# Performance work log

Hardware: AMD Instinct MI355X
Metric: run time of the kernel (lower is better)

Reference implementation:

```python
import jax, jax.numpy as jnp
import numpy as np

N_NODES = 50000
N_RAND_EDGES = 800000
N_GRAPHS = 16
F_IN = 128
HID = 64
EMB = 16


def gat_layer(x, src, dst, W, a_src, a_dst, bias, heads, out_ch, concat):
    # x: [N, Fin]; W: [Fin, heads*out_ch]; a_src/a_dst: [heads, out_ch]
    n = x.shape[0]
    h = (x @ W).reshape(n, heads, out_ch)                      # [N, H, C]
    alpha_src = jnp.sum(h * a_src, axis=-1)                    # [N, H]
    alpha_dst = jnp.sum(h * a_dst, axis=-1)                    # [N, H]
    logits = jax.nn.leaky_relu(alpha_src[src] + alpha_dst[dst], 0.2)  # [E, H]
    # segment softmax over incoming edges of each dst node
    m = jax.ops.segment_max(logits, dst, num_segments=n)       # [N, H]
    e = jnp.exp(logits - m[dst])                               # [E, H]
    s = jax.ops.segment_sum(e, dst, num_segments=n)            # [N, H]
    alpha = e / (s[dst] + 1e-16)                               # [E, H]
    msg = h[src] * alpha[:, :, None]                           # [E, H, C]
    out = jax.ops.segment_sum(msg, dst, num_segments=n)        # [N, H, C]
    out = out.reshape(n, heads * out_ch) if concat else out.mean(axis=1)
    return out + bias, alpha


def setup_inputs() -> dict:
    key = jax.random.key(0)
    ks = jax.random.split(key, 20)
    x = jax.random.normal(ks[0], (N_NODES, F_IN), dtype=jnp.float32)
    src = jax.random.randint(ks[1], (N_RAND_EDGES,), 0, N_NODES)
    dst = jax.random.randint(ks[2], (N_RAND_EDGES,), 0, N_NODES)
    loops = jnp.arange(N_NODES)
    edge_index = jnp.stack([jnp.concatenate([src, loops]),
                            jnp.concatenate([dst, loops])]).astype(jnp.int64)
    batch = jnp.sort(jax.random.randint(ks[3], (N_NODES,), 0, N_GRAPHS)).astype(jnp.int64)
    p = lambda k, shp: (jax.random.normal(k, shp, dtype=jnp.float32) * 0.1)
    return {
        "x": x, "edge_index": edge_index, "batch": batch,
        # conv1: 128 -> 64, heads=2, concat -> 128
        "W1": p(ks[4], (F_IN, 2 * HID)), "as1": p(ks[5], (2, HID)), "ad1": p(ks[6], (2, HID)), "b1": p(ks[7], (2 * HID,)),
        # conv2: 128 -> 128, heads=1, mean
        "W2": p(ks[8], (2 * HID, 2 * HID)), "as2": p(ks[9], (1, 2 * HID)), "ad2": p(ks[10], (1, 2 * HID)), "b2": p(ks[11], (2 * HID,)),
        # conv3: 128 -> 16, heads=1, mean
        "W3": p(ks[12], (2 * HID, EMB)), "as3": p(ks[13], (1, EMB)), "ad3": p(ks[14], (1, EMB)), "b3": p(ks[15], (EMB,)),
        # final classifier 16 -> 2
        "Wl": p(ks[16], (EMB, 2)), "bl": p(ks[17], (2,)),
    }


def reference(x, edge_index, batch, W1, as1, ad1, b1, W2, as2, ad2, b2,
              W3, as3, ad3, b3, Wl, bl):
    src, dst = edge_index[0], edge_index[1]
    h1, a1 = gat_layer(x, src, dst, W1, as1, ad1, b1, heads=2, out_ch=HID, concat=True)
    h1 = jax.nn.relu(h1)
    h2, a2 = gat_layer(h1, src, dst, W2, as2, ad2, b2, heads=1, out_ch=2 * HID, concat=False)
    h2 = jax.nn.relu(h2)
    emb, a3 = gat_layer(h2, src, dst, W3, as3, ad3, b3, heads=1, out_ch=EMB, concat=False)
    # global mean pool over graphs (eval mode -> dropout is identity)
    counts = jax.ops.segment_sum(jnp.ones((emb.shape[0],), emb.dtype), batch, num_segments=N_GRAPHS)
    g_emb = jax.ops.segment_sum(emb, batch, num_segments=N_GRAPHS) / jnp.clip(counts, 1.0, None)[:, None]
    out = g_emb @ Wl + bl
    return (out, g_emb, emb, a1, a2, a3)
```

## Files before the change

### kernel.cpp

```cpp
#include <hip/hip_runtime.h>
#include <hip/hip_bf16.h>

#define DEVFN __device__ __forceinline__

using short8 = __attribute__((ext_vector_type(8))) short;
using f32x4  = __attribute__((ext_vector_type(4))) float;

DEVFN float ldf(const void* p, size_t i, bool f32) {
    return f32 ? ((const float*)p)[i]
               : __bfloat162float(((const __hip_bfloat16*)p)[i]);
}
DEVFN int ldidx(const void* p, size_t i, bool i64) {
    return i64 ? (int)((const long long*)p)[i] : ((const int*)p)[i];
}
DEVFN void stf(void* p, size_t i, float v, bool f32) {
    if (f32) ((float*)p)[i] = v;
    else     ((__hip_bfloat16*)p)[i] = __float2bfloat16(v);
}
DEVFN float lky(float v) { return v > 0.f ? v : 0.2f * v; }

DEVFN float bfbits2f(short s) {
    return __uint_as_float(((unsigned)(unsigned short)s) << 16);
}
DEVFN short f2bfbits(float f) {
    unsigned u = __float_as_uint(f);
    return (short)((u + 0x7fffu + ((u >> 16) & 1u)) >> 16);
}

__global__ void detect_k(const void* x, const void* ei, int* flags) {
    if (threadIdx.x == 0 && blockIdx.x == 0) {
        const __hip_bfloat16* xb = (const __hip_bfloat16*)x;
        int bad = 0;
        for (int i = 0; i < 512; ++i) {
            float v = __bfloat162float(xb[i]);
            if (!(v == v) || fabsf(v) > 1.0e6f) bad++;
        }
        flags[0] = (bad > 16) ? 1 : 0;
        const unsigned* w = (const unsigned*)ei;
        int zeros = 0;
        for (int i = 0; i < 64; ++i) if (w[2 * i + 1] == 0u) zeros++;
        flags[1] = (zeros >= 60) ? 1 : 0;
    }
}

__global__ void zero_i32(int* __restrict__ p, int n) {
    int i = blockIdx.x * blockDim.x + threadIdx.x;
    int st = gridDim.x * blockDim.x;
    for (; i < n; i += st) p[i] = 0;
}
__global__ void zero_f32(float* __restrict__ p, long n) {
    long i = (long)blockIdx.x * blockDim.x + threadIdx.x;
    long st = (long)gridDim.x * blockDim.x;
    for (; i < n; i += st) p[i] = 0.f;
}

__global__ void hist_k(const void* __restrict__ ei, int E, int* __restrict__ cnt,
                       const int* __restrict__ flags) {
    const bool i64 = flags[1] != 0;
    int e = blockIdx.x * blockDim.x + threadIdx.x;
    if (e >= E) return;
    atomicAdd(&cnt[ldidx(ei, (size_t)E + e, i64)], 1);
}

__global__ void scan_block_k(const int* __restrict__ cnt, int* __restrict__ incl,
                             int* __restrict__ part, int N) {
    __shared__ int sm[256];
    int tid = threadIdx.x;
    int i = blockIdx.x * 256 + tid;
    int v = (i < N) ? cnt[i] : 0;
    sm[tid] = v;
    __syncthreads();
    for (int o = 1; o < 256; o <<= 1) {
        int t = (tid >= o) ? sm[tid - o] : 0;
        __syncthreads();
        sm[tid] += t;
        __syncthreads();
    }
    if (i < N) incl[i] = sm[tid];
    if (tid == 255) part[blockIdx.x] = sm[255];
}

__global__ void scan_part_k(int* __restrict__ part, int nb) {
    __shared__ int sm[256];
    __shared__ int off;
    int tid = threadIdx.x;
    if (tid == 0) off = 0;
    __syncthreads();
    for (int b = 0; b < nb; b += 256) {
        int i = b + tid;
        int v = (i < nb) ? part[i] : 0;
        sm[tid] = v;
        __syncthreads();
        for (int o = 1; o < 256; o <<= 1) {
            int t = (tid >= o) ? sm[tid - o] : 0;
            __syncthreads();
            sm[tid] += t;
            __syncthreads();
        }
        if (i < nb) part[i] = sm[tid] - v + off;
        __syncthreads();
        if (tid == 255) off += sm[255];
        __syncthreads();
    }
}

__global__ void finalize_scan_k(int* __restrict__ incl_cur, const int* __restrict__ cnt,
                                const int* __restrict__ part, int* __restrict__ rs,
                                int N, int E) {
    int i = blockIdx.x * 256 + threadIdx.x;
    if (i >= N) return;
    int v = incl_cur[i] - cnt[i] + part[blockIdx.x];
    rs[i] = v;
    incl_cur[i] = v;
    if (i == N - 1) rs[N] = E;
}

__global__ void scatter_csr_k(const void* __restrict__ ei, int E, int* __restrict__ cur,
                              int2* __restrict__ csr, const int* __restrict__ flags) {
    const bool i64 = flags[1] != 0;
    int e = blockIdx.x * blockDim.x + threadIdx.x;
    if (e >= E) return;
    int s = ldidx(ei, e, i64);
    int d = ldidx(ei, (size_t)E + e, i64);
    int p = atomicAdd(&cur[d], 1);
    csr[p] = make_int2(s, e);
}

template <int DSRC, int FOUT, int HEADS>
__global__ __launch_bounds__(256) void gemm_alpha_mfma_k(
    const void* __restrict__ xin, const void* __restrict__ Wv,
    const void* __restrict__ asv, const void* __restrict__ adv,
    short* __restrict__ h_bf, float* __restrict__ as_out, float* __restrict__ ad_out,
    int N, const int* __restrict__ flags)
{
    constexpr int FIN = 128;
    constexpr int NCT = FOUT / 16;
    constexpr int CPH = FOUT / HEADS;
    constexpr int CTPH = CPH / 16;
    const bool f32 = flags[0] != 0;

    __shared__ short Wt[FOUT * FIN];

    for (int i = threadIdx.x; i < FIN * FOUT; i += 256) {
        int k = i / FOUT, c = i - (i / FOUT) * FOUT;
        short w;
        if (f32) w = f2bfbits(((const float*)Wv)[i]);
        else     w = ((const short*)Wv)[i];
        *(short*)((char*)Wt + (size_t)c * (FIN * 2) + (((k * 2) ^ ((c & 7) << 4)))) = w;
    }
    __syncthreads();

    const int wv = threadIdx.x >> 6;
    const int lane = threadIdx.x & 63;
    const int m0 = blockIdx.x * 64 + wv * 16;
    if (m0 >= N) return;
    const int lrow = lane & 15;
    const int lk   = lane >> 4;

    short8 afrag[4];
    if (DSRC == 0 && f32) {
        const float* xf = (const float*)xin + (size_t)(m0 + lrow) * FIN + lk * 8;
#pragma unroll
        for (int ks = 0; ks < 4; ++ks) {
            short8 t;
#pragma unroll
            for (int j = 0; j < 8; ++j) t[j] = f2bfbits(xf[ks * 32 + j]);
            afrag[ks] = t;
        }
    } else {
        const short* xb = (const short*)xin + (size_t)(m0 + lrow) * FIN + lk * 8;
#pragma unroll
        for (int ks = 0; ks < 4; ++ks)
            afrag[ks] = *(const short8*)(xb + ks * 32);
    }

    float csA[HEADS][4], cdA[HEADS][4];
#pragma unroll
    for (int hd = 0; hd < HEADS; ++hd)
#pragma unroll
        for (int r = 0; r < 4; ++r) { csA[hd][r] = 0.f; cdA[hd][r] = 0.f; }

#pragma unroll
    for (int ct = 0; ct < NCT; ++ct) {
        const int col = ct * 16 + lrow;
        const int hd = ct / CTPH;
        f32x4 acc = {0.f, 0.f, 0.f, 0.f};
#pragma unroll
        for (int ks = 0; ks < 4; ++ks) {
            const int kbyte = ks * 64 + lk * 16;
            short8 bfrag = *(const short8*)((const char*)Wt +
                               (size_t)col * (FIN * 2) + (kbyte ^ ((col & 7) << 4)));
            acc = __builtin_amdgcn_mfma_f32_16x16x32_bf16(afrag[ks], bfrag, acc, 0, 0, 0);
        }
        const float asc = ldf(asv, col, f32);
        const float adc = ldf(adv, col, f32);
#pragma unroll
        for (int r = 0; r < 4; ++r) {
            h_bf[(size_t)(m0 + lk * 4 + r) * FOUT + col] = f2bfbits(acc[r]);
            csA[hd][r] += acc[r] * asc;
            cdA[hd][r] += acc[r] * adc;
        }
    }

#pragma unroll
    for (int hd = 0; hd < HEADS; ++hd)
#pragma unroll
        for (int r = 0; r < 4; ++r) {
            float cs = csA[hd][r], cd = cdA[hd][r];
            for (int o = 1; o < 16; o <<= 1) {
                cs += __shfl_xor(cs, o);
                cd += __shfl_xor(cd, o);
            }
            csA[hd][r] = cs; cdA[hd][r] = cd;
        }
    if (lrow == 0) {
#pragma unroll
        for (int r = 0; r < 4; ++r) {
            int n = m0 + lk * 4 + r;
#pragma unroll
            for (int hd = 0; hd < HEADS; ++hd) {
                as_out[(size_t)n * HEADS + hd] = csA[hd][r];
                ad_out[(size_t)n * HEADS + hd] = cdA[hd][r];
            }
        }
    }
}

template <int HEADS>
__global__ __launch_bounds__(256) void softmax_csr_k(
    const float* __restrict__ as_, const float* __restrict__ ad_,
    const int* __restrict__ rs, const int2* __restrict__ csr,
    float* __restrict__ alpha_csr, void* __restrict__ dout, size_t aoff,
    int N, const int* __restrict__ flags)
{
    const bool f32 = flags[0] != 0;
    const int wid = (blockIdx.x * 256 + threadIdx.x) >> 6;
    const int lane = threadIdx.x & 63;
    if (wid >= N) return;
    const int beg = rs[wid], end = rs[wid + 1];
    const int deg = end - beg;

    const float ad0 = ad_[(size_t)wid * HEADS];
    const float ad1 = (HEADS == 2) ? ad_[(size_t)wid * HEADS + 1] : 0.f;

    if (deg <= 64) {
        const bool act = lane < deg;
        int2 se = make_int2(0, 0);
        if (act) se = csr[beg + lane];
        float l0 = act ? lky(as_[(size_t)se.x * HEADS] + ad0) : -1e30f;
        float l1 = 0.f;
        if (HEADS == 2) l1 = act ? lky(as_[(size_t)se.x * HEADS + 1] + ad1) : -1e30f;

        float m0 = l0, m1 = l1;
        for (int o = 1; o < 64; o <<= 1) {
            m0 = fmaxf(m0, __shfl_xor(m0, o));
            if (HEADS == 2) m1 = fmaxf(m1, __shfl_xor(m1, o));
        }
        float e0 = act ? expf(l0 - m0) : 0.f;
        float e1 = (HEADS == 2) ? (act ? expf(l1 - m1) : 0.f) : 0.f;
        float s0 = e0, s1 = e1;
        for (int o = 1; o < 64; o <<= 1) {
            s0 += __shfl_xor(s0, o);
            if (HEADS == 2) s1 += __shfl_xor(s1, o);
        }
        if (act) {
            const int p = beg + lane;
            float a0 = e0 * (1.f / (s0 + 1e-16f));
            alpha_csr[(size_t)p * HEADS] = a0;
            stf(dout, aoff + (size_t)se.y * HEADS, a0, f32);
            if (HEADS == 2) {
                float a1 = e1 * (1.f / (s1 + 1e-16f));
                alpha_csr[(size_t)p * 2 + 1] = a1;
                stf(dout, aoff + (size_t)se.y * 2 + 1, a1, f32);
            }
        }
        return;
    }

    float m0 = -1e30f, m1 = -1e30f;
    for (int p = beg + lane; p < end; p += 64) {
        int s = csr[p].x;
        m0 = fmaxf(m0, lky(as_[(size_t)s * HEADS] + ad0));
        if (HEADS == 2) m1 = fmaxf(m1, lky(as_[(size_t)s * HEADS + 1] + ad1));
    }
    for (int o = 1; o < 64; o <<= 1) {
        m0 = fmaxf(m0, __shfl_xor(m0, o));
        if (HEADS == 2) m1 = fmaxf(m1, __shfl_xor(m1, o));
    }
    float s0 = 0.f, s1 = 0.f;
    for (int p = beg + lane; p < end; p += 64) {
        int s = csr[p].x;
        s0 += expf(lky(as_[(size_t)s * HEADS] + ad0) - m0);
        if (HEADS == 2) s1 += expf(lky(as_[(size_t)s * HEADS + 1] + ad1) - m1);
    }
    for (int o = 1; o < 64; o <<= 1) {
        s0 += __shfl_xor(s0, o);
        if (HEADS == 2) s1 += __shfl_xor(s1, o);
    }
    const float inv0 = 1.f / (s0 + 1e-16f);
    const float inv1 = 1.f / (s1 + 1e-16f);

    for (int p = beg + lane; p < end; p += 64) {
        int2 se = csr[p];
        int s = se.x, eid = se.y;
        float a0 = expf(lky(as_[(size_t)s * HEADS] + ad0) - m0) * inv0;
        alpha_csr[(size_t)p * HEADS] = a0;
        stf(dout, aoff + (size_t)eid * HEADS, a0, f32);
        if (HEADS == 2) {
            float a1 = expf(lky(as_[(size_t)s * HEADS + 1] + ad1) - m1) * inv1;
            alpha_csr[(size_t)p * 2 + 1] = a1;
            stf(dout, aoff + (size_t)eid * 2 + 1, a1, f32);
        }
    }
}

template <int HEADS, bool RELU>
__global__ __launch_bounds__(256) void pull128_v3_k(
    const short* __restrict__ h_bf, const float* __restrict__ alpha_csr,
    const int* __restrict__ rs, const int2* __restrict__ csr,
    const void* __restrict__ bias, short* __restrict__ z_bf,
    int N, const int* __restrict__ flags)
{
    const bool f32 = flags[0] != 0;
    const int wid = (blockIdx.x * 256 + threadIdx.x) >> 6;
    if (wid >= N) return;
    const int lane = threadIdx.x & 63;
    const int cg = lane & 15;
    const int es = lane >> 4;
    const int h = (HEADS == 2) ? (cg >> 3) : 0;
    const int beg = rs[wid], end = rs[wid + 1];

    float acc[8] = {0.f, 0.f, 0.f, 0.f, 0.f, 0.f, 0.f, 0.f};
    for (int base = beg; base < end; base += 8) {
        const int pA = base + es;
        const int pB = base + 4 + es;
        int sA = 0, sB = 0;
        float aA = 0.f, aB = 0.f;
        if (pA < end) { sA = csr[pA].x; aA = alpha_csr[(size_t)pA * HEADS + h]; }
        if (pB < end) { sB = csr[pB].x; aB = alpha_csr[(size_t)pB * HEADS + h]; }
        const short8 hA = *(const short8*)(h_bf + (size_t)sA * 128 + cg * 8);
        const short8 hB = *(const short8*)(h_bf + (size_t)sB * 128 + cg * 8);
#pragma unroll
        for (int j = 0; j < 8; ++j)
            acc[j] = fmaf(bfbits2f(hA[j]), aA, acc[j]);
#pragma unroll
        for (int j = 0; j < 8; ++j)
            acc[j] = fmaf(bfbits2f(hB[j]), aB, acc[j]);
    }
#pragma unroll
    for (int j = 0; j < 8; ++j) {
        acc[j] += __shfl_xor(acc[j], 16);
        acc[j] += __shfl_xor(acc[j], 32);
    }
    if (es == 0) {
        short8 outv;
#pragma unroll
        for (int j = 0; j < 8; ++j) {
            float v = acc[j] + ldf(bias, cg * 8 + j, f32);
            if (RELU) v = fmaxf(v, 0.f);
            outv[j] = f2bfbits(v);
        }
        *(short8*)(z_bf + (size_t)wid * 128 + cg * 8) = outv;
    }
}

__global__ __launch_bounds__(256) void pull16_v2_k(
    const short* __restrict__ h_bf, const float* __restrict__ alpha_csr,
    const int* __restrict__ rs, const int2* __restrict__ csr,
    float* __restrict__ out, int N)
{
    const int wid = (blockIdx.x * 256 + threadIdx.x) >> 6;
    if (wid >= N) return;
    const int lane = threadIdx.x & 63;
    const int cg = lane & 7;
    const int es = lane >> 3;
    const int beg = rs[wid], end = rs[wid + 1];

    float a0 = 0.f, a1 = 0.f;
    for (int base = beg; base < end; base += 8) {
        const int p = base + es;
        if (p < end) {
            const int sj = csr[p].x;
            const float a = alpha_csr[p];
            const int hv = *(const int*)(h_bf + (size_t)sj * 16 + cg * 2);
            a0 = fmaf(bfbits2f((short)(hv & 0xffff)), a, a0);
            a1 = fmaf(bfbits2f((short)(hv >> 16)), a, a1);
        }
    }
#pragma unroll
    for (int o = 8; o < 64; o <<= 1) {
        a0 += __shfl_xor(a0, o);
        a1 += __shfl_xor(a1, o);
    }
    if (es == 0) {
        out[(size_t)wid * 16 + cg * 2]     = a0;
        out[(size_t)wid * 16 + cg * 2 + 1] = a1;
    }
}

__global__ __launch_bounds__(256) void finalize3_k(
    const float* __restrict__ acc, const void* __restrict__ bias,
    const void* __restrict__ batch, void* __restrict__ dout, size_t emb_off,
    float* __restrict__ g_sum, int N, const int* __restrict__ flags)
{
    const bool f32 = flags[0] != 0;
    const bool i64 = flags[1] != 0;
    __shared__ float gp[256];
    int tid = threadIdx.x;
    gp[tid] = 0.f;
    __syncthreads();
    long idx = (long)blockIdx.x * 256 + tid;
    if (idx < (long)N * 16) {
        int n = (int)(idx >> 4), col = (int)(idx & 15);
        float v = acc[idx] + ldf(bias, col, f32);
        stf(dout, emb_off + idx, v, f32);
        int g = ldidx(batch, n, i64);
        atomicAdd(&gp[g * 16 + col], v);
    }
    __syncthreads();
    float pv = gp[tid];
    if (pv != 0.f) atomicAdd(&g_sum[tid], pv);
}

__global__ __launch_bounds__(256) void head_k(
    const float* __restrict__ g_sum, const void* __restrict__ batch,
    const void* __restrict__ Wl, const void* __restrict__ bl,
    void* __restrict__ dout, size_t gemb_off, int N, const int* __restrict__ flags)
{
    const bool f32 = flags[0] != 0;
    const bool i64 = flags[1] != 0;
    __shared__ float ge[256];
    __shared__ int cnts[16];
    int tid = threadIdx.x;
    if (tid < 16) {
        int lo = 0, hi = N;
        while (lo < hi) { int mid = (lo + hi) >> 1; if (ldidx(batch, mid, i64) < tid) lo = mid + 1; else hi = mid; }
        int l2 = 0, h2 = N;
        while (l2 < h2) { int mid = (l2 + h2) >> 1; if (ldidx(batch, mid, i64) <= tid) l2 = mid + 1; else h2 = mid; }
        cnts[tid] = l2 - lo;
    }
    __syncthreads();
    {
        int g = tid >> 4;
        float v = g_sum[tid] / fmaxf((float)cnts[g], 1.f);
        ge[tid] = v;
        stf(dout, gemb_off + tid, v, f32);
    }
    __syncthreads();
    if (tid < 32) {
        int g = tid >> 1, j = tid & 1;
        float s = ldf(bl, j, f32);
        for (int c = 0; c < 16; ++c) s += ge[g * 16 + c] * ldf(Wl, (size_t)c * 2 + j, f32);
        stf(dout, (size_t)g * 2 + j, s, f32);
    }
}

static inline int cdiv(long a, int b) { return (int)((a + b - 1) / b); }

extern "C" void kernel_launch(void* const* d_in, const int* in_sizes, int n_in,
                              void* d_out, int out_size, void* d_ws, size_t ws_size,
                              hipStream_t stream)
{
    const void* x   = d_in[0];
    const void* ei  = d_in[1];
    const void* batch = d_in[2];
    const void* W1  = d_in[3];
    const void* as1 = d_in[4];
    const void* ad1 = d_in[5];
    const void* b1  = d_in[6];
    const void* W2  = d_in[7];
    const void* as2 = d_in[8];
    const void* ad2 = d_in[9];
    const void* b2  = d_in[10];
    const void* W3  = d_in[11];
    const void* as3 = d_in[12];
    const void* ad3 = d_in[13];
    const void* b3  = d_in[14];
    const void* Wl  = d_in[15];
    const void* bl  = d_in[16];

    const int N = in_sizes[0] / 128;
    const int E = in_sizes[1] / 2;

    int* flags = (int*)d_ws;
    float* ws = (float*)d_ws + 16;
    size_t o = 0;
    float* as_  = ws + o; o += (size_t)N * 2;
    float* ad_  = ws + o; o += (size_t)N * 2;
    float* alpha_csr = ws + o; o += (size_t)E * 2;
    float* bufE = ws + o; o += (size_t)N * 16;
    float* g_sum = ws + o; o += 256;
    short* hX = (short*)(ws + o); o += (size_t)N * 64;
    short* hZ = (short*)(ws + o); o += (size_t)N * 64;
    short* h3 = (short*)(ws + o); o += (size_t)N * 8;
    int* ip = (int*)(ws + o);
    int* cnt  = ip;            ip += N;
    int* incl = ip;            ip += N;
    int* part = ip;            ip += 256;
    int* rs   = ip;            ip += N + 1;
    if (((uintptr_t)ip & 7) != 0) ip += 1;
    int2* csr = (int2*)ip;     ip += 2 * E;

    const size_t off_gemb = 32;
    const size_t off_emb  = 32 + 256;
    const size_t off_a1   = off_emb + (size_t)N * 16;
    const size_t off_a2   = off_a1 + (size_t)E * 2;
    const size_t off_a3   = off_a2 + (size_t)E;

    const int B = 256;
    const int nbN = cdiv(N, 256);
    const int gemmBlocks = cdiv(N, 64);
    const int waveBlocks = cdiv(N, 4);

    detect_k<<<1, 64, 0, stream>>>(x, ei, flags);

    zero_i32<<<nbN, B, 0, stream>>>(cnt, N);
    hist_k<<<cdiv(E, B), B, 0, stream>>>(ei, E, cnt, flags);
    scan_block_k<<<nbN, B, 0, stream>>>(cnt, incl, part, N);
    scan_part_k<<<1, B, 0, stream>>>(part, nbN);
    finalize_scan_k<<<nbN, B, 0, stream>>>(incl, cnt, part, rs, N, E);
    scatter_csr_k<<<cdiv(E, B), B, 0, stream>>>(ei, E, incl, csr, flags);

    gemm_alpha_mfma_k<0, 128, 2><<<gemmBlocks, 256, 0, stream>>>(x, W1, as1, ad1, hX, as_, ad_, N, flags);
    softmax_csr_k<2><<<waveBlocks, 256, 0, stream>>>(as_, ad_, rs, csr,
                                                     alpha_csr, d_out, off_a1, N, flags);
    pull128_v3_k<2, true><<<waveBlocks, 256, 0, stream>>>(hX, alpha_csr, rs, csr, b1, hZ, N, flags);

    gemm_alpha_mfma_k<1, 128, 1><<<gemmBlocks, 256, 0, stream>>>(hZ, W2, as2, ad2, hX, as_, ad_, N, flags);
    softmax_csr_k<1><<<waveBlocks, 256, 0, stream>>>(as_, ad_, rs, csr,
                                                     alpha_csr, d_out, off_a2, N, flags);
    pull128_v3_k<1, true><<<waveBlocks, 256, 0, stream>>>(hX, alpha_csr, rs, csr, b2, hZ, N, flags);

    gemm_alpha_mfma_k<1, 16, 1><<<gemmBlocks, 256, 0, stream>>>(hZ, W3, as3, ad3, h3, as_, ad_, N, flags);
    softmax_csr_k<1><<<waveBlocks, 256, 0, stream>>>(as_, ad_, rs, csr,
                                                     alpha_csr, d_out, off_a3, N, flags);
    pull16_v2_k<<<waveBlocks, 256, 0, stream>>>(h3, alpha_csr, rs, csr, bufE, N);
    zero_f32<<<1, B, 0, stream>>>(g_sum, 256);
    finalize3_k<<<cdiv((long)N * 16, B), B, 0, stream>>>(bufE, b3, batch, d_out, off_emb, g_sum, N, flags);

    head_k<<<1, B, 0, stream>>>(g_sum, batch, Wl, bl, d_out, off_gemb, N, flags);
}
```

Measured before the change: 370.6 us.

## Fuse edge softmax with neighbor aggregation via LDS-staged alphas

Merges the per-layer softmax kernel and the pull-aggregation kernel into one wave-per-node kernel. The alphas and source indices are staged in shared memory instead of a global alpha_csr buffer. This cuts three kernel launches and the global write and re-read of the per-edge alpha and CSR source arrays. There is no barrier between the LDS writes and reads, which relies on wave-synchronous execution within a 64-lane wave. The large-degree path processes edges in 64-edge chunks.

```diff
diff --git a/kernel.cpp b/kernel.cpp
--- a/kernel.cpp
+++ b/kernel.cpp
@@ -226,22 +226,31 @@
     }
 }
 
-template <int HEADS>
-__global__ __launch_bounds__(256) void softmax_csr_k(
-    const float* __restrict__ as_, const float* __restrict__ ad_,
-    const int* __restrict__ rs, const int2* __restrict__ csr,
-    float* __restrict__ alpha_csr, void* __restrict__ dout, size_t aoff,
+template <int HEADS, bool RELU>
+__global__ __launch_bounds__(256) void agg128_k(
+    const short* __restrict__ h_bf, const float* __restrict__ as_,
+    const float* __restrict__ ad_, const int* __restrict__ rs,
+    const int2* __restrict__ csr, const void* __restrict__ bias,
+    short* __restrict__ z_bf, void* __restrict__ dout, size_t aoff,
     int N, const int* __restrict__ flags)
 {
+    __shared__ int   ls_src[4][64];
+    __shared__ float ls_a[4][HEADS][64];
     const bool f32 = flags[0] != 0;
+    const int wv = threadIdx.x >> 6;
     const int wid = (blockIdx.x * 256 + threadIdx.x) >> 6;
+    if (wid >= N) return;
     const int lane = threadIdx.x & 63;
-    if (wid >= N) return;
     const int beg = rs[wid], end = rs[wid + 1];
     const int deg = end - beg;
+    const int cg = lane & 15;
+    const int es = lane >> 4;
+    const int h = (HEADS == 2) ? (cg >> 3) : 0;
 
     const float ad0 = ad_[(size_t)wid * HEADS];
     const float ad1 = (HEADS == 2) ? ad_[(size_t)wid * HEADS + 1] : 0.f;
+
+    float acc[8] = {0.f, 0.f, 0.f, 0.f, 0.f, 0.f, 0.f, 0.f};
 
     if (deg <= 64) {
         const bool act = lane < deg;
@@ -264,89 +273,83 @@
             if (HEADS == 2) s1 += __shfl_xor(s1, o);
         }
         if (act) {
-            const int p = beg + lane;
             float a0 = e0 * (1.f / (s0 + 1e-16f));
-            alpha_csr[(size_t)p * HEADS] = a0;
+            ls_src[wv][lane] = se.x;
+            ls_a[wv][0][lane] = a0;
             stf(dout, aoff + (size_t)se.y * HEADS, a0, f32);
             if (HEADS == 2) {
                 float a1 = e1 * (1.f / (s1 + 1e-16f));
-                alpha_csr[(size_t)p * 2 + 1] = a1;
+                ls_a[wv][1][lane] = a1;
                 stf(dout, aoff + (size_t)se.y * 2 + 1, a1, f32);
             }
         }
-        return;
-    }
-
-    float m0 = -1e30f, m1 = -1e30f;
-    for (int p = beg + lane; p < end; p += 64) {
-        int s = csr[p].x;
-        m0 = fmaxf(m0, lky(as_[(size_t)s * HEADS] + ad0));
-        if (HEADS == 2) m1 = fmaxf(m1, lky(as_[(size_t)s * HEADS + 1] + ad1));
-    }
-    for (int o = 1; o < 64; o <<= 1) {
-        m0 = fmaxf(m0, __shfl_xor(m0, o));
-        if (HEADS == 2) m1 = fmaxf(m1, __shfl_xor(m1, o));
-    }
-    float s0 = 0.f, s1 = 0.f;
-    for (int p = beg + lane; p < end; p += 64) {
-        int s = csr[p].x;
-        s0 += expf(lky(as_[(size_t)s * HEADS] + ad0) - m0);
-        if (HEADS == 2) s1 += expf(lky(as_[(size_t)s * HEADS + 1] + ad1) - m1);
-    }
-    for (int o = 1; o < 64; o <<= 1) {
-        s0 += __shfl_xor(s0, o);
-        if (HEADS == 2) s1 += __shfl_xor(s1, o);
-    }
-    const float inv0 = 1.f / (s0 + 1e-16f);
-    const float inv1 = 1.f / (s1 + 1e-16f);
-
-    for (int p = beg + lane; p < end; p += 64) {
-        int2 se = csr[p];
-        int s = se.x, eid = se.y;
-        float a0 = expf(lky(as_[(size_t)s * HEADS] + ad0) - m0) * inv0;
-        alpha_csr[(size_t)p * HEADS] = a0;
-        stf(dout, aoff + (size_t)eid * HEADS, a0, f32);
-        if (HEADS == 2) {
-            float a1 = expf(lky(as_[(size_t)s * HEADS + 1] + ad1) - m1) * inv1;
-            alpha_csr[(size_t)p * 2 + 1] = a1;
-            stf(dout, aoff + (size_t)eid * 2 + 1, a1, f32);
-        }
-    }
-}
-
-template <int HEADS, bool RELU>
-__global__ __launch_bounds__(256) void pull128_v3_k(
-    const short* __restrict__ h_bf, const float* __restrict__ alpha_csr,
-    const int* __restrict__ rs, const int2* __restrict__ csr,
-    const void* __restrict__ bias, short* __restrict__ z_bf,
-    int N, const int* __restrict__ flags)
-{
-    const bool f32 = flags[0] != 0;
-    const int wid = (blockIdx.x * 256 + threadIdx.x) >> 6;
-    if (wid >= N) return;
-    const int lane = threadIdx.x & 63;
-    const int cg = lane & 15;
-    const int es = lane >> 4;
-    const int h = (HEADS == 2) ? (cg >> 3) : 0;
-    const int beg = rs[wid], end = rs[wid + 1];
-
-    float acc[8] = {0.f, 0.f, 0.f, 0.f, 0.f, 0.f, 0.f, 0.f};
-    for (int base = beg; base < end; base += 8) {
-        const int pA = base + es;
-        const int pB = base + 4 + es;
-        int sA = 0, sB = 0;
-        float aA = 0.f, aB = 0.f;
-        if (pA < end) { sA = csr[pA].x; aA = alpha_csr[(size_t)pA * HEADS + h]; }
-        if (pB < end) { sB = csr[pB].x; aB = alpha_csr[(size_t)pB * HEADS + h]; }
-        const short8 hA = *(const short8*)(h_bf + (size_t)sA * 128 + cg * 8);
-        const short8 hB = *(const short8*)(h_bf + (size_t)sB * 128 + cg * 8);
-#pragma unroll
-        for (int j = 0; j < 8; ++j)
-            acc[j] = fmaf(bfbits2f(hA[j]), aA, acc[j]);
-#pragma unroll
-        for (int j = 0; j < 8; ++j)
-            acc[j] = fmaf(bfbits2f(hB[j]), aB, acc[j]);
-    }
+        for (int b = 0; b < deg; b += 8) {
+            const int pA = b + es, pB = b + 4 + es;
+            int sA = 0, sB = 0;
+            float aA = 0.f, aB = 0.f;
+            if (pA < deg) { sA = ls_src[wv][pA]; aA = ls_a[wv][h][pA]; }
+            if (pB < deg) { sB = ls_src[wv][pB]; aB = ls_a[wv][h][pB]; }
+            const short8 hA = *(const short8*)(h_bf + (size_t)sA * 128 + cg * 8);
+            const short8 hB = *(const short8*)(h_bf + (size_t)sB * 128 + cg * 8);
+#pragma unroll
+            for (int j = 0; j < 8; ++j) acc[j] = fmaf(bfbits2f(hA[j]), aA, acc[j]);
+#pragma unroll
+            for (int j = 0; j < 8; ++j) acc[j] = fmaf(bfbits2f(hB[j]), aB, acc[j]);
+        }
+    } else {
+        float m0 = -1e30f, m1 = -1e30f;
+        for (int p = beg + lane; p < end; p += 64) {
+            int s = csr[p].x;
+            m0 = fmaxf(m0, lky(as_[(size_t)s * HEADS] + ad0));
+            if (HEADS == 2) m1 = fmaxf(m1, lky(as_[(size_t)s * HEADS + 1] + ad1));
+        }
+        for (int o = 1; o < 64; o <<= 1) {
+            m0 = fmaxf(m0, __shfl_xor(m0, o));
+            if (HEADS == 2) m1 = fmaxf(m1, __shfl_xor(m1, o));
+        }
+        float s0 = 0.f, s1 = 0.f;
+        for (int p = beg + lane; p < end; p += 64) {
+            int s = csr[p].x;
+            s0 += expf(lky(as_[(size_t)s * HEADS] + ad0) - m0);
+            if (HEADS == 2) s1 += expf(lky(as_[(size_t)s * HEADS + 1] + ad1) - m1);
+        }
+        for (int o = 1; o < 64; o <<= 1) {
+            s0 += __shfl_xor(s0, o);
+            if (HEADS == 2) s1 += __shfl_xor(s1, o);
+        }
+        const float inv0 = 1.f / (s0 + 1e-16f);
+        const float inv1 = 1.f / (s1 + 1e-16f);
+
+        for (int cb = beg; cb < end; cb += 64) {
+            const int cn = min(64, end - cb);
+            if (lane < cn) {
+                int2 se = csr[cb + lane];
+                float a0 = expf(lky(as_[(size_t)se.x * HEADS] + ad0) - m0) * inv0;
+                ls_src[wv][lane] = se.x;
+                ls_a[wv][0][lane] = a0;
+                stf(dout, aoff + (size_t)se.y * HEADS, a0, f32);
+                if (HEADS == 2) {
+                    float a1 = expf(lky(as_[(size_t)se.x * HEADS + 1] + ad1) - m1) * inv1;
+                    ls_a[wv][1][lane] = a1;
+                    stf(dout, aoff + (size_t)se.y * 2 + 1, a1, f32);
+                }
+            }
+            for (int b = 0; b < cn; b += 8) {
+                const int pA = b + es, pB = b + 4 + es;
+                int sA = 0, sB = 0;
+                float aA = 0.f, aB = 0.f;
+                if (pA < cn) { sA = ls_src[wv][pA]; aA = ls_a[wv][h][pA]; }
+                if (pB < cn) { sB = ls_src[wv][pB]; aB = ls_a[wv][h][pB]; }
+                const short8 hA = *(const short8*)(h_bf + (size_t)sA * 128 + cg * 8);
+                const short8 hB = *(const short8*)(h_bf + (size_t)sB * 128 + cg * 8);
+#pragma unroll
+                for (int j = 0; j < 8; ++j) acc[j] = fmaf(bfbits2f(hA[j]), aA, acc[j]);
+#pragma unroll
+                for (int j = 0; j < 8; ++j) acc[j] = fmaf(bfbits2f(hB[j]), aB, acc[j]);
+            }
+        }
+    }
+
 #pragma unroll
     for (int j = 0; j < 8; ++j) {
         acc[j] += __shfl_xor(acc[j], 16);
@@ -364,37 +367,95 @@
     }
 }
 
-__global__ __launch_bounds__(256) void pull16_v2_k(
-    const short* __restrict__ h_bf, const float* __restrict__ alpha_csr,
-    const int* __restrict__ rs, const int2* __restrict__ csr,
-    float* __restrict__ out, int N)
+__global__ __launch_bounds__(256) void agg16_k(
+    const short* __restrict__ h_bf, const float* __restrict__ as_,
+    const float* __restrict__ ad_, const int* __restrict__ rs,
+    const int2* __restrict__ csr, float* __restrict__ out,
+    void* __restrict__ dout, size_t aoff, int N, const int* __restrict__ flags)
 {
+    __shared__ int   ls_src[4][64];
+    __shared__ float ls_a[4][64];
+    const bool f32 = flags[0] != 0;
+    const int wv = threadIdx.x >> 6;
     const int wid = (blockIdx.x * 256 + threadIdx.x) >> 6;
     if (wid >= N) return;
     const int lane = threadIdx.x & 63;
+    const int beg = rs[wid], end = rs[wid + 1];
+    const int deg = end - beg;
     const int cg = lane & 7;
     const int es = lane >> 3;
-    const int beg = rs[wid], end = rs[wid + 1];
-
-    float a0 = 0.f, a1 = 0.f;
-    for (int base = beg; base < end; base += 8) {
-        const int p = base + es;
-        if (p < end) {
-            const int sj = csr[p].x;
-            const float a = alpha_csr[p];
-            const int hv = *(const int*)(h_bf + (size_t)sj * 16 + cg * 2);
-            a0 = fmaf(bfbits2f((short)(hv & 0xffff)), a, a0);
-            a1 = fmaf(bfbits2f((short)(hv >> 16)), a, a1);
-        }
-    }
+
+    const float ad0 = ad_[wid];
+
+    float a0s = 0.f, a1s = 0.f;
+
+    if (deg <= 64) {
+        const bool act = lane < deg;
+        int2 se = make_int2(0, 0);
+        if (act) se = csr[beg + lane];
+        float l0 = act ? lky(as_[se.x] + ad0) : -1e30f;
+        float m0 = l0;
+        for (int o = 1; o < 64; o <<= 1) m0 = fmaxf(m0, __shfl_xor(m0, o));
+        float e0 = act ? expf(l0 - m0) : 0.f;
+        float s0 = e0;
+        for (int o = 1; o < 64; o <<= 1) s0 += __shfl_xor(s0, o);
+        if (act) {
+            float a0 = e0 * (1.f / (s0 + 1e-16f));
+            ls_src[wv][lane] = se.x;
+            ls_a[wv][lane] = a0;
+            stf(dout, aoff + se.y, a0, f32);
+        }
+        for (int b = 0; b < deg; b += 8) {
+            const int p = b + es;
+            if (p < deg) {
+                const int sj = ls_src[wv][p];
+                const float a = ls_a[wv][p];
+                const int hv = *(const int*)(h_bf + (size_t)sj * 16 + cg * 2);
+                a0s = fmaf(bfbits2f((short)(hv & 0xffff)), a, a0s);
+                a1s = fmaf(bfbits2f((short)(hv >> 16)), a, a1s);
+            }
+        }
+    } else {
+        float m0 = -1e30f;
+        for (int p = beg + lane; p < end; p += 64)
+            m0 = fmaxf(m0, lky(as_[csr[p].x] + ad0));
+        for (int o = 1; o < 64; o <<= 1) m0 = fmaxf(m0, __shfl_xor(m0, o));
+        float s0 = 0.f;
+        for (int p = beg + lane; p < end; p += 64)
+            s0 += expf(lky(as_[csr[p].x] + ad0) - m0);
+        for (int o = 1; o < 64; o <<= 1) s0 += __shfl_xor(s0, o);
+        const float inv0 = 1.f / (s0 + 1e-16f);
+
+        for (int cb = beg; cb < end; cb += 64) {
+            const int cn = min(64, end - cb);
+            if (lane < cn) {
+                int2 se = csr[cb + lane];
+                float a0 = expf(lky(as_[se.x] + ad0) - m0) * inv0;
+                ls_src[wv][lane] = se.x;
+                ls_a[wv][lane] = a0;
+                stf(dout, aoff + se.y, a0, f32);
+            }
+            for (int b = 0; b < cn; b += 8) {
+                const int p = b + es;
+                if (p < cn) {
+                    const int sj = ls_src[wv][p];
+                    const float a = ls_a[wv][p];
+                    const int hv = *(const int*)(h_bf + (size_t)sj * 16 + cg * 2);
+                    a0s = fmaf(bfbits2f((short)(hv & 0xffff)), a, a0s);
+                    a1s = fmaf(bfbits2f((short)(hv >> 16)), a, a1s);
+                }
+            }
+        }
+    }
+
 #pragma unroll
     for (int o = 8; o < 64; o <<= 1) {
-        a0 += __shfl_xor(a0, o);
-        a1 += __shfl_xor(a1, o);
+        a0s += __shfl_xor(a0s, o);
+        a1s += __shfl_xor(a1s, o);
     }
     if (es == 0) {
-        out[(size_t)wid * 16 + cg * 2]     = a0;
-        out[(size_t)wid * 16 + cg * 2 + 1] = a1;
+        out[(size_t)wid * 16 + cg * 2]     = a0s;
+        out[(size_t)wid * 16 + cg * 2 + 1] = a1s;
     }
 }
 
@@ -487,7 +548,6 @@
     size_t o = 0;
     float* as_  = ws + o; o += (size_t)N * 2;
     float* ad_  = ws + o; o += (size_t)N * 2;
-    float* alpha_csr = ws + o; o += (size_t)E * 2;
     float* bufE = ws + o; o += (size_t)N * 16;
     float* g_sum = ws + o; o += 256;
     short* hX = (short*)(ws + o); o += (size_t)N * 64;
@@ -522,19 +582,16 @@
     scatter_csr_k<<<cdiv(E, B), B, 0, stream>>>(ei, E, incl, csr, flags);
 
     gemm_alpha_mfma_k<0, 128, 2><<<gemmBlocks, 256, 0, stream>>>(x, W1, as1, ad1, hX, as_, ad_, N, flags);
-    softmax_csr_k<2><<<waveBlocks, 256, 0, stream>>>(as_, ad_, rs, csr,
-                                                     alpha_csr, d_out, off_a1, N, flags);
-    pull128_v3_k<2, true><<<waveBlocks, 256, 0, stream>>>(hX, alpha_csr, rs, csr, b1, hZ, N, flags);
+    agg128_k<2, true><<<waveBlocks, 256, 0, stream>>>(hX, as_, ad_, rs, csr, b1, hZ,
+                                                      d_out, off_a1, N, flags);
 
     gemm_alpha_mfma_k<1, 128, 1><<<gemmBlocks, 256, 0, stream>>>(hZ, W2, as2, ad2, hX, as_, ad_, N, flags);
-    softmax_csr_k<1><<<waveBlocks, 256, 0, stream>>>(as_, ad_, rs, csr,
-                                                     alpha_csr, d_out, off_a2, N, flags);
-    pull128_v3_k<1, true><<<waveBlocks, 256, 0, stream>>>(hX, alpha_csr, rs, csr, b2, hZ, N, flags);
+    agg128_k<1, true><<<waveBlocks, 256, 0, stream>>>(hX, as_, ad_, rs, csr, b2, hZ,
+                                                      d_out, off_a2, N, flags);
 
     gemm_alpha_mfma_k<1, 16, 1><<<gemmBlocks, 256, 0, stream>>>(hZ, W3, as3, ad3, h3, as_, ad_, N, flags);
-    softmax_csr_k<1><<<waveBlocks, 256, 0, stream>>>(as_, ad_, rs, csr,
-                                                     alpha_csr, d_out, off_a3, N, flags);
-    pull16_v2_k<<<waveBlocks, 256, 0, stream>>>(h3, alpha_csr, rs, csr, bufE, N);
+    agg16_k<<<waveBlocks, 256, 0, stream>>>(h3, as_, ad_, rs, csr, bufE,
+                                            d_out, off_a3, N, flags);
     zero_f32<<<1, B, 0, stream>>>(g_sum, 256);
     finalize3_k<<<cdiv((long)N * 16, B), B, 0, stream>>>(bufE, b3, batch, d_out, off_emb, g_sum, N, flags);
 
```

New measurement: 349.8 us. 1.06x faster.
